# Kernel optimization log

Measured on AMD Instinct MI355X. Metric: run time of the kernel, lower is better.

Reference implementation:

```python
import jax, jax.numpy as jnp
import numpy as np

B, N, D = 4, 2048, 512   # batch, seq, feed_forward_size
H, DK, DV = 8, 64, 64    # heads, key_dim, value_dim
LN_EPS = 1e-5


def setup_inputs() -> dict:
    key = jax.random.key(0)
    ks = jax.random.split(key, 12)
    s = 0.02
    x = jax.random.normal(ks[0], (B, N, D), dtype=jnp.float32)
    # boolean mask, True = masked out (torch masked_fill semantics); causal
    attn_mask = ~jnp.tril(jnp.ones((N, N), dtype=bool))[None, None]
    ln_g = jnp.ones((D,), jnp.float32)
    ln_b = jnp.zeros((D,), jnp.float32)
    wq = jax.random.normal(ks[1], (D, H * DK), jnp.float32) * s
    bq = jnp.zeros((H * DK,), jnp.float32)
    wk = jax.random.normal(ks[2], (D, H * DK), jnp.float32) * s
    bk = jnp.zeros((H * DK,), jnp.float32)
    wv = jax.random.normal(ks[3], (D, H * DV), jnp.float32) * s
    bv = jnp.zeros((H * DV,), jnp.float32)
    wo = jax.random.normal(ks[4], (H * DV, D), jnp.float32) * s
    bo = jnp.zeros((D,), jnp.float32)
    return {"x": x, "attn_mask": attn_mask, "ln_g": ln_g, "ln_b": ln_b,
            "wq": wq, "bq": bq, "wk": wk, "bk": bk, "wv": wv, "bv": bv,
            "wo": wo, "bo": bo}


def _layernorm(x, g, b):
    mu = jnp.mean(x, axis=-1, keepdims=True)
    var = jnp.mean(jnp.square(x - mu), axis=-1, keepdims=True)
    return (x - mu) * jax.lax.rsqrt(var + LN_EPS) * g + b


def reference(x, attn_mask, ln_g, ln_b, wq, bq, wk, bk, wv, bv, wo, bo):
    xn = _layernorm(x, ln_g, ln_b)
    scale = DK ** -0.5
    q = (xn @ wq + bq).reshape(B, N, H, DK).transpose(0, 2, 1, 3) * scale  # b h n d
    k = (xn @ wk + bk).reshape(B, N, H, DK).transpose(0, 2, 1, 3)
    v = (xn @ wv + bv).reshape(B, N, H, DV).transpose(0, 2, 1, 3)
    sim = jnp.einsum('bhid,bhjd->bhij', q, k)
    sim = jnp.where(attn_mask, -jnp.finfo(sim.dtype).max, sim)
    attn = jax.nn.softmax(sim, axis=-1)  # dropout p=0 (eval)
    out = jnp.einsum('bhij,bhjd->bhid', attn, v)
    out = out.transpose(0, 2, 1, 3).reshape(B, N, H * DV)  # b n (h d)
    return out @ wo + bo
```

## Files before the change

kernel.cpp:

```cpp
#include <hip/hip_runtime.h>

typedef unsigned short u16;
typedef unsigned long long u64;
typedef __bf16 bf16x8 __attribute__((ext_vector_type(8)));
typedef float f32x4 __attribute__((ext_vector_type(4)));
typedef float f32x16 __attribute__((ext_vector_type(16)));

#define H_HEADS 8
#define DHEAD 64
#define NSEQ 2048
#define DMODEL 512
#define BATCH 4
#define MROWS (BATCH * NSEQ)
#define BH (BATCH * H_HEADS)

__device__ __forceinline__ u16 f2bf(float f) {
  unsigned u = __builtin_bit_cast(unsigned, f);
  u += 0x7fffu + ((u >> 16) & 1u);
  return (u16)(u >> 16);
}

__device__ __forceinline__ bf16x8 ldfrag(const u16* p) {
  return __builtin_bit_cast(bf16x8, *(const uint4*)p);
}

typedef __attribute__((address_space(1))) void GV;
typedef __attribute__((address_space(3))) void LV;
__device__ __forceinline__ void gld16(const void* g, void* l) {
  __builtin_amdgcn_global_load_lds((GV*)g, (LV*)l, 16, 0, 0);
}

__global__ __launch_bounds__(256) void ln_kernel(
    const float* __restrict__ x, const float* __restrict__ g,
    const float* __restrict__ b, u16* __restrict__ xn) {
  const int row = blockIdx.x;
  const int t = threadIdx.x;
  const float2 v = *(const float2*)(x + (size_t)row * DMODEL + t * 2);
  float s = v.x + v.y;
  float ss = v.x * v.x + v.y * v.y;
  #pragma unroll
  for (int d = 1; d < 64; d <<= 1) {
    s += __shfl_xor(s, d);
    ss += __shfl_xor(ss, d);
  }
  __shared__ float red[8];
  const int wave = t >> 6, lane = t & 63;
  if (lane == 0) { red[wave] = s; red[4 + wave] = ss; }
  __syncthreads();
  s = red[0] + red[1] + red[2] + red[3];
  ss = red[4] + red[5] + red[6] + red[7];
  const float mean = s * (1.0f / DMODEL);
  const float var = ss * (1.0f / DMODEL) - mean * mean;
  const float rstd = rsqrtf(var + 1e-5f);
  const float2 gg = *(const float2*)(g + t * 2);
  const float2 bb = *(const float2*)(b + t * 2);
  const float o0 = (v.x - mean) * rstd * gg.x + bb.x;
  const float o1 = (v.y - mean) * rstd * gg.y + bb.y;
  const unsigned packed = (unsigned)f2bf(o0) | ((unsigned)f2bf(o1) << 16);
  *(unsigned*)(xn + (size_t)row * DMODEL + t * 2) = packed;
}

__global__ __launch_bounds__(256) void transpose_w4_kernel(
    const float* __restrict__ w0, const float* __restrict__ w1,
    const float* __restrict__ w2, const float* __restrict__ w3,
    u16* __restrict__ WT) {
  __shared__ float tile[32][33];
  const int z = blockIdx.z;
  const float* W = (z == 0) ? w0 : (z == 1) ? w1 : (z == 2) ? w2 : w3;
  u16* dst = WT + (size_t)z * DMODEL * DMODEL;
  const int n0 = blockIdx.x * 32, k0 = blockIdx.y * 32;
  const int t = threadIdx.x;
  #pragma unroll
  for (int p = 0; p < 4; ++p) {
    const int u = p * 256 + t;
    const int r = u >> 5, c = u & 31;
    tile[r][c] = W[(size_t)(k0 + r) * DMODEL + n0 + c];
  }
  __syncthreads();
  #pragma unroll
  for (int p = 0; p < 4; ++p) {
    const int u = p * 256 + t;
    const int rn = u >> 5, ck = u & 31;
    dst[(size_t)(n0 + rn) * DMODEL + k0 + ck] = f2bf(tile[ck][rn]);
  }
}

template <int MODE>
__global__ __launch_bounds__(256) void gemm128_kernel(
    const u16* __restrict__ A, const u16* __restrict__ BT,
    const float* __restrict__ bq, const float* __restrict__ bk,
    const float* __restrict__ bv,
    u16* __restrict__ qb, u16* __restrict__ kb, u16* __restrict__ vtb,
    float* __restrict__ fout, int K) {
  __shared__ u16 lds_a[128 * 64];
  __shared__ u16 lds_b[128 * 64];
  const int t = threadIdx.x;
  const int lane = t & 63, wave = t >> 6;
  const int wm = wave >> 1, wn = wave & 1;
  const int lo = lane & 15, hi = lane >> 4;
  const int m0 = blockIdx.y * 128, n0 = blockIdx.x * 128;
  const int sr = lane >> 3;
  const int scol = (((lane & 7) ^ sr) * 8);
  f32x4 acc[4][4] = {};
  for (int k0 = 0; k0 < K; k0 += 64) {
    #pragma unroll
    for (int j = 0; j < 4; ++j) {
      const int ch = wave * 4 + j;
      gld16(A + (size_t)(m0 + ch * 8 + sr) * K + k0 + scol, lds_a + ch * 512);
      gld16(BT + (size_t)(n0 + ch * 8 + sr) * K + k0 + scol, lds_b + ch * 512);
    }
    __syncthreads();
    #pragma unroll
    for (int kc = 0; kc < 2; ++kc) {
      bf16x8 af[4], bfr[4];
      const int sw = ((lo & 7) * 8);
      #pragma unroll
      for (int i = 0; i < 4; ++i)
        af[i] = ldfrag(lds_a + (wm * 64 + i * 16 + lo) * 64 + ((kc * 32 + hi * 8) ^ sw));
      #pragma unroll
      for (int i = 0; i < 4; ++i)
        bfr[i] = ldfrag(lds_b + (wn * 64 + i * 16 + lo) * 64 + ((kc * 32 + hi * 8) ^ sw));
      __builtin_amdgcn_s_setprio(1);
      #pragma unroll
      for (int mi = 0; mi < 4; ++mi)
        #pragma unroll
        for (int ni = 0; ni < 4; ++ni)
          acc[mi][ni] = __builtin_amdgcn_mfma_f32_16x16x32_bf16(
              af[mi], bfr[ni], acc[mi][ni], 0, 0, 0);
      __builtin_amdgcn_s_setprio(0);
    }
    __syncthreads();
  }
  #pragma unroll
  for (int mi = 0; mi < 4; ++mi) {
    #pragma unroll
    for (int ni = 0; ni < 4; ++ni) {
      const int col = n0 + wn * 64 + ni * 16 + lo;
      if (MODE == 0) {
        const int mat = col >> 9, w = col & 511;
        const int hh = w >> 6, dk = w & 63;
        const float bi = (mat == 0 ? bq : (mat == 1 ? bk : bv))[w];
        const int row0 = m0 + wm * 64 + mi * 16 + hi * 4;
        const int bbx = row0 >> 11, seq0 = row0 & 2047;
        if (mat == 2) {
          u64 pk = 0;
          #pragma unroll
          for (int r = 0; r < 4; ++r)
            pk |= (u64)f2bf(acc[mi][ni][r] + bi) << (16 * r);
          *(u64*)(vtb + ((size_t)(bbx * H_HEADS + hh) * DHEAD + dk) * NSEQ + seq0) = pk;
        } else {
          const float sc = (mat == 0) ? 0.18033688f : 1.0f;
          u16* dst = (mat == 0 ? qb : kb);
          #pragma unroll
          for (int r = 0; r < 4; ++r)
            dst[(((size_t)(bbx * H_HEADS + hh) * NSEQ) + seq0 + r) * DHEAD + dk] =
                f2bf((acc[mi][ni][r] + bi) * sc);
        }
      } else {
        const float bi = bq[col];
        #pragma unroll
        for (int r = 0; r < 4; ++r) {
          const int row = m0 + wm * 64 + mi * 16 + hi * 4 + r;
          fout[(size_t)row * DMODEL + col] = acc[mi][ni][r] + bi;
        }
      }
    }
  }
}

__global__ __launch_bounds__(256, 2) void attn_kernel(
    const u16* __restrict__ Q, const u16* __restrict__ K,
    const u16* __restrict__ VT, u16* __restrict__ O) {
  __shared__ u16 lds_k[2][4096];
  __shared__ u16 lds_v[2][4096];
  const int t = threadIdx.x;
  const int lane = t & 63, wave = t >> 6;
  const int l31 = lane & 31, hi = lane >> 5;
  const int l7 = lane & 7;

  const int n = blockIdx.x;
  const int s_id = n >> 8, g = n & 255;
  const int u_id = g >> 4, q_id = g & 15;
  const int ist = (s_id & 1) ? (15 - q_id) : q_id;
  const int bh = u_id + 16 * s_id;
  const int b = bh >> 3, h = bh & 7;

  const u16* Qh = Q + (size_t)bh * NSEQ * DHEAD;
  const u16* Kh = K + (size_t)bh * NSEQ * DHEAD;
  const u16* Vh = VT + (size_t)bh * DHEAD * NSEQ;

  const int q0w = ist * 128 + wave * 32;
  const int nt = 2 * ist + 2;
  const int lastkt = (q0w + 31) >> 6;
  const int qrow = q0w + l31;

  bf16x8 qf[4];
  #pragma unroll
  for (int c = 0; c < 4; ++c)
    qf[c] = ldfrag(Qh + (size_t)qrow * DHEAD + c * 16 + hi * 8);

  f32x16 o0 = {}, o1 = {};
  float m = -INFINITY, l = 0.0f;

  const int sr = lane >> 3;
  const int scol = ((lane & 7) ^ sr) * 8;
  const int swz = l7 * 8;

  #pragma unroll
  for (int j = 0; j < 2; ++j) {
    const int ch = wave * 2 + j;
    gld16(Kh + (size_t)(ch * 8 + sr) * DHEAD + scol, lds_k[0] + ch * 512);
    gld16(Vh + (size_t)(ch * 8 + sr) * NSEQ + scol, lds_v[0] + ch * 512);
  }

  for (int kt = 0; kt < nt; ++kt) {
    const int cur = kt & 1;
    if (kt + 1 < nt) {
      const int kvn = (kt + 1) * 64;
      #pragma unroll
      for (int j = 0; j < 2; ++j) {
        const int ch = wave * 2 + j;
        gld16(Kh + (size_t)(kvn + ch * 8 + sr) * DHEAD + scol, lds_k[cur ^ 1] + ch * 512);
        gld16(Vh + (size_t)(ch * 8 + sr) * NSEQ + kvn + scol, lds_v[cur ^ 1] + ch * 512);
      }
      asm volatile("s_waitcnt vmcnt(4)" ::: "memory");
    } else {
      asm volatile("s_waitcnt vmcnt(0)" ::: "memory");
    }
    __builtin_amdgcn_s_barrier();
    __builtin_amdgcn_sched_barrier(0);

    if (kt <= lastkt) {
      const u16* lk = lds_k[cur];
      const u16* lv = lds_v[cur];
      f32x16 st0 = {}, st1 = {};

      __builtin_amdgcn_s_setprio(1);
      #pragma unroll
      for (int c = 0; c < 4; ++c) {
        const int col = (c * 16 + hi * 8) ^ swz;
        bf16x8 kf0 = ldfrag(lk + l31 * 64 + col);
        bf16x8 kf1 = ldfrag(lk + (32 + l31) * 64 + col);
        st0 = __builtin_amdgcn_mfma_f32_32x32x16_bf16(kf0, qf[c], st0, 0, 0, 0);
        st1 = __builtin_amdgcn_mfma_f32_32x32x16_bf16(kf1, qf[c], st1, 0, 0, 0);
      }
      __builtin_amdgcn_s_setprio(0);

      if (kt == lastkt) {
        const int kvb = kt * 64 + 4 * hi;
        #pragma unroll
        for (int r = 0; r < 16; ++r) {
          const int kv = kvb + (r & 3) + 8 * (r >> 2);
          if (kv > qrow) st0[r] = -1e30f;
          if (kv + 32 > qrow) st1[r] = -1e30f;
        }
      }

      float pm = st0[0];
      #pragma unroll
      for (int r = 1; r < 16; ++r) pm = fmaxf(pm, st0[r]);
      #pragma unroll
      for (int r = 0; r < 16; ++r) pm = fmaxf(pm, st1[r]);
      pm = fmaxf(pm, __shfl_xor(pm, 32));
      const float mn = fmaxf(m, pm);
      const float sc = exp2f(m - mn);
      m = mn;
      float ps = 0.0f;
      #pragma unroll
      for (int r = 0; r < 16; ++r) { st0[r] = exp2f(st0[r] - mn); ps += st0[r]; }
      #pragma unroll
      for (int r = 0; r < 16; ++r) { st1[r] = exp2f(st1[r] - mn); ps += st1[r]; }
      ps += __shfl_xor(ps, 32);
      l = l * sc + ps;
      #pragma unroll
      for (int r = 0; r < 16; ++r) { o0[r] *= sc; o1[r] *= sc; }

      bf16x8 pf0, pf1, pf2, pf3;
      {
        unsigned w0, w1, w2, w3, w4, w5, w6, w7;
        asm("v_cvt_pk_bf16_f32 %0, %1, %2" : "=v"(w0) : "v"(st0[0]), "v"(st0[1]));
        asm("v_cvt_pk_bf16_f32 %0, %1, %2" : "=v"(w1) : "v"(st0[2]), "v"(st0[3]));
        asm("v_cvt_pk_bf16_f32 %0, %1, %2" : "=v"(w2) : "v"(st0[4]), "v"(st0[5]));
        asm("v_cvt_pk_bf16_f32 %0, %1, %2" : "=v"(w3) : "v"(st0[6]), "v"(st0[7]));
        asm("v_cvt_pk_bf16_f32 %0, %1, %2" : "=v"(w4) : "v"(st0[8]), "v"(st0[9]));
        asm("v_cvt_pk_bf16_f32 %0, %1, %2" : "=v"(w5) : "v"(st0[10]), "v"(st0[11]));
        asm("v_cvt_pk_bf16_f32 %0, %1, %2" : "=v"(w6) : "v"(st0[12]), "v"(st0[13]));
        asm("v_cvt_pk_bf16_f32 %0, %1, %2" : "=v"(w7) : "v"(st0[14]), "v"(st0[15]));
        asm("v_permlane32_swap_b32 %0, %1" : "+v"(w0), "+v"(w2));
        asm("v_permlane32_swap_b32 %0, %1" : "+v"(w1), "+v"(w3));
        asm("v_permlane32_swap_b32 %0, %1" : "+v"(w4), "+v"(w6));
        asm("v_permlane32_swap_b32 %0, %1" : "+v"(w5), "+v"(w7));
        union Uu { unsigned u[4]; bf16x8 v; };
        Uu a; a.u[0] = w0; a.u[1] = w1; a.u[2] = w2; a.u[3] = w3; pf0 = a.v;
        Uu bb; bb.u[0] = w4; bb.u[1] = w5; bb.u[2] = w6; bb.u[3] = w7; pf1 = bb.v;
      }
      {
        unsigned w0, w1, w2, w3, w4, w5, w6, w7;
        asm("v_cvt_pk_bf16_f32 %0, %1, %2" : "=v"(w0) : "v"(st1[0]), "v"(st1[1]));
        asm("v_cvt_pk_bf16_f32 %0, %1, %2" : "=v"(w1) : "v"(st1[2]), "v"(st1[3]));
        asm("v_cvt_pk_bf16_f32 %0, %1, %2" : "=v"(w2) : "v"(st1[4]), "v"(st1[5]));
        asm("v_cvt_pk_bf16_f32 %0, %1, %2" : "=v"(w3) : "v"(st1[6]), "v"(st1[7]));
        asm("v_cvt_pk_bf16_f32 %0, %1, %2" : "=v"(w4) : "v"(st1[8]), "v"(st1[9]));
        asm("v_cvt_pk_bf16_f32 %0, %1, %2" : "=v"(w5) : "v"(st1[10]), "v"(st1[11]));
        asm("v_cvt_pk_bf16_f32 %0, %1, %2" : "=v"(w6) : "v"(st1[12]), "v"(st1[13]));
        asm("v_cvt_pk_bf16_f32 %0, %1, %2" : "=v"(w7) : "v"(st1[14]), "v"(st1[15]));
        asm("v_permlane32_swap_b32 %0, %1" : "+v"(w0), "+v"(w2));
        asm("v_permlane32_swap_b32 %0, %1" : "+v"(w1), "+v"(w3));
        asm("v_permlane32_swap_b32 %0, %1" : "+v"(w4), "+v"(w6));
        asm("v_permlane32_swap_b32 %0, %1" : "+v"(w5), "+v"(w7));
        union Uu { unsigned u[4]; bf16x8 v; };
        Uu a; a.u[0] = w0; a.u[1] = w1; a.u[2] = w2; a.u[3] = w3; pf2 = a.v;
        Uu bb; bb.u[0] = w4; bb.u[1] = w5; bb.u[2] = w6; bb.u[3] = w7; pf3 = bb.v;
      }

      __builtin_amdgcn_s_setprio(1);
      #pragma unroll
      for (int c = 0; c < 4; ++c) {
        const int col = (c * 16 + hi * 8) ^ swz;
        bf16x8 vf0 = ldfrag(lv + l31 * 64 + col);
        bf16x8 vf1 = ldfrag(lv + (32 + l31) * 64 + col);
        const bf16x8 pc = (c == 0) ? pf0 : (c == 1) ? pf1 : (c == 2) ? pf2 : pf3;
        o0 = __builtin_amdgcn_mfma_f32_32x32x16_bf16(vf0, pc, o0, 0, 0, 0);
        o1 = __builtin_amdgcn_mfma_f32_32x32x16_bf16(vf1, pc, o1, 0, 0, 0);
      }
      __builtin_amdgcn_s_setprio(0);
    }
    __builtin_amdgcn_sched_barrier(0);
    __builtin_amdgcn_s_barrier();
    __builtin_amdgcn_sched_barrier(0);
  }

  const float rl = __builtin_amdgcn_rcpf(l);
  u16* Ob = O + ((size_t)b * NSEQ + qrow) * DMODEL + h * DHEAD;
  #pragma unroll
  for (int d = 0; d < 2; ++d) {
    #pragma unroll
    for (int mq = 0; mq < 4; ++mq) {
      u64 pk = 0;
      #pragma unroll
      for (int c3 = 0; c3 < 4; ++c3) {
        const float v = (d ? o1[mq * 4 + c3] : o0[mq * 4 + c3]) * rl;
        pk |= (u64)f2bf(v) << (16 * c3);
      }
      *(u64*)(Ob + d * 32 + mq * 8 + hi * 4) = pk;
    }
  }
}

extern "C" void kernel_launch(void* const* d_in, const int* in_sizes, int n_in,
                              void* d_out, int out_size, void* d_ws, size_t ws_size,
                              hipStream_t stream) {
  const float* x = (const float*)d_in[0];
  const float* ln_g = (const float*)d_in[2];
  const float* ln_b = (const float*)d_in[3];
  const float* wq = (const float*)d_in[4];
  const float* bq = (const float*)d_in[5];
  const float* wk = (const float*)d_in[6];
  const float* bk = (const float*)d_in[7];
  const float* wv = (const float*)d_in[8];
  const float* bv = (const float*)d_in[9];
  const float* wo = (const float*)d_in[10];
  const float* bo = (const float*)d_in[11];

  char* ws = (char*)d_ws;
  u16* xn = (u16*)ws;     ws += (size_t)MROWS * DMODEL * 2;
  u16* wqkvT = (u16*)ws;  ws += (size_t)4 * DMODEL * DMODEL * 2;
  u16* woT = wqkvT + (size_t)3 * DMODEL * DMODEL;
  u16* qb = (u16*)ws;     ws += (size_t)MROWS * DMODEL * 2;
  u16* kb = (u16*)ws;     ws += (size_t)MROWS * DMODEL * 2;
  u16* vtb = (u16*)ws;    ws += (size_t)MROWS * DMODEL * 2;
  u16* attnb = (u16*)ws;  ws += (size_t)MROWS * DMODEL * 2;

  ln_kernel<<<MROWS, 256, 0, stream>>>(x, ln_g, ln_b, xn);
  transpose_w4_kernel<<<dim3(16, 16, 4), 256, 0, stream>>>(wq, wk, wv, wo, wqkvT);

  gemm128_kernel<0><<<dim3(12, 64), 256, 0, stream>>>(
      xn, wqkvT, bq, bk, bv, qb, kb, vtb, nullptr, DMODEL);

  attn_kernel<<<512, 256, 0, stream>>>(qb, kb, vtb, attnb);

  gemm128_kernel<1><<<dim3(4, 64), 256, 0, stream>>>(
      attnb, woT, bo, nullptr, nullptr, nullptr, nullptr, nullptr,
      (float*)d_out, DMODEL);
}
```

Before: 111.6 us.

## Split causal attention along KV into chunks with a separate merge kernel

Each causal query tile's KV range is split into up to four chunks of eight KV tiles, so the grid grows from 512 to 1280 blocks of roughly equal work. Tiles with more than one chunk write unnormalised fp32 partial outputs plus running max and sum to workspace, and a new merge kernel combines them into the bf16 attention output. Launch bounds are raised to allow four blocks per CU. The goal is better load balance and occupancy on the causal triangle. The cost is extra fp32 traffic for the partials, an additional kernel launch, and possible register pressure from the tighter launch bound.

```diff
diff --git a/kernel.cpp b/kernel.cpp
--- a/kernel.cpp
+++ b/kernel.cpp
@@ -168,9 +168,10 @@
   }
 }
 
-__global__ __launch_bounds__(256, 2) void attn_kernel(
+__global__ __launch_bounds__(256, 4) void attn_kernel(
     const u16* __restrict__ Q, const u16* __restrict__ K,
-    const u16* __restrict__ VT, u16* __restrict__ O) {
+    const u16* __restrict__ VT, u16* __restrict__ O,
+    float* __restrict__ pO, float* __restrict__ pML) {
   __shared__ u16 lds_k[2][4096];
   __shared__ u16 lds_v[2][4096];
   const int t = threadIdx.x;
@@ -179,18 +180,23 @@
   const int l7 = lane & 7;
 
   const int n = blockIdx.x;
-  const int s_id = n >> 8, g = n & 255;
-  const int u_id = g >> 4, q_id = g & 15;
-  const int ist = (s_id & 1) ? (15 - q_id) : q_id;
-  const int bh = u_id + 16 * s_id;
+  const int bh = n / 40;
+  const int r = n % 40;
+  int qt, ck, C;
+  if (r < 4)       { qt = r;                 C = 1; ck = 0; }
+  else if (r < 12) { qt = 4 + ((r - 4) >> 1);  C = 2; ck = (r - 4) & 1; }
+  else if (r < 24) { qt = 8 + (r - 12) / 3;    C = 3; ck = (r - 12) % 3; }
+  else             { qt = 12 + ((r - 24) >> 2); C = 4; ck = (r - 24) & 3; }
+  const int T = 2 * qt + 2;
+  const int kc0 = ck * 8;
+  const int L = min(8, T - kc0);
+
   const int b = bh >> 3, h = bh & 7;
-
   const u16* Qh = Q + (size_t)bh * NSEQ * DHEAD;
   const u16* Kh = K + (size_t)bh * NSEQ * DHEAD;
   const u16* Vh = VT + (size_t)bh * DHEAD * NSEQ;
 
-  const int q0w = ist * 128 + wave * 32;
-  const int nt = 2 * ist + 2;
+  const int q0w = qt * 128 + wave * 32;
   const int lastkt = (q0w + 31) >> 6;
   const int qrow = q0w + l31;
 
@@ -209,14 +215,15 @@
   #pragma unroll
   for (int j = 0; j < 2; ++j) {
     const int ch = wave * 2 + j;
-    gld16(Kh + (size_t)(ch * 8 + sr) * DHEAD + scol, lds_k[0] + ch * 512);
-    gld16(Vh + (size_t)(ch * 8 + sr) * NSEQ + scol, lds_v[0] + ch * 512);
-  }
-
-  for (int kt = 0; kt < nt; ++kt) {
-    const int cur = kt & 1;
-    if (kt + 1 < nt) {
-      const int kvn = (kt + 1) * 64;
+    gld16(Kh + (size_t)(kc0 * 64 + ch * 8 + sr) * DHEAD + scol, lds_k[0] + ch * 512);
+    gld16(Vh + (size_t)(ch * 8 + sr) * NSEQ + kc0 * 64 + scol, lds_v[0] + ch * 512);
+  }
+
+  for (int lt = 0; lt < L; ++lt) {
+    const int gk = kc0 + lt;
+    const int cur = lt & 1;
+    if (lt + 1 < L) {
+      const int kvn = (gk + 1) * 64;
       #pragma unroll
       for (int j = 0; j < 2; ++j) {
         const int ch = wave * 2 + j;
@@ -230,7 +237,7 @@
     __builtin_amdgcn_s_barrier();
     __builtin_amdgcn_sched_barrier(0);
 
-    if (kt <= lastkt) {
+    if (gk <= lastkt) {
       const u16* lk = lds_k[cur];
       const u16* lv = lds_v[cur];
       f32x16 st0 = {}, st1 = {};
@@ -246,34 +253,34 @@
       }
       __builtin_amdgcn_s_setprio(0);
 
-      if (kt == lastkt) {
-        const int kvb = kt * 64 + 4 * hi;
+      if (gk == lastkt) {
+        const int kvb = gk * 64 + 4 * hi;
         #pragma unroll
-        for (int r = 0; r < 16; ++r) {
-          const int kv = kvb + (r & 3) + 8 * (r >> 2);
-          if (kv > qrow) st0[r] = -1e30f;
-          if (kv + 32 > qrow) st1[r] = -1e30f;
+        for (int rr = 0; rr < 16; ++rr) {
+          const int kv = kvb + (rr & 3) + 8 * (rr >> 2);
+          if (kv > qrow) st0[rr] = -1e30f;
+          if (kv + 32 > qrow) st1[rr] = -1e30f;
         }
       }
 
       float pm = st0[0];
       #pragma unroll
-      for (int r = 1; r < 16; ++r) pm = fmaxf(pm, st0[r]);
-      #pragma unroll
-      for (int r = 0; r < 16; ++r) pm = fmaxf(pm, st1[r]);
+      for (int rr = 1; rr < 16; ++rr) pm = fmaxf(pm, st0[rr]);
+      #pragma unroll
+      for (int rr = 0; rr < 16; ++rr) pm = fmaxf(pm, st1[rr]);
       pm = fmaxf(pm, __shfl_xor(pm, 32));
       const float mn = fmaxf(m, pm);
       const float sc = exp2f(m - mn);
       m = mn;
       float ps = 0.0f;
       #pragma unroll
-      for (int r = 0; r < 16; ++r) { st0[r] = exp2f(st0[r] - mn); ps += st0[r]; }
-      #pragma unroll
-      for (int r = 0; r < 16; ++r) { st1[r] = exp2f(st1[r] - mn); ps += st1[r]; }
+      for (int rr = 0; rr < 16; ++rr) { st0[rr] = exp2f(st0[rr] - mn); ps += st0[rr]; }
+      #pragma unroll
+      for (int rr = 0; rr < 16; ++rr) { st1[rr] = exp2f(st1[rr] - mn); ps += st1[rr]; }
       ps += __shfl_xor(ps, 32);
       l = l * sc + ps;
       #pragma unroll
-      for (int r = 0; r < 16; ++r) { o0[r] *= sc; o1[r] *= sc; }
+      for (int rr = 0; rr < 16; ++rr) { o0[rr] *= sc; o1[rr] *= sc; }
 
       bf16x8 pf0, pf1, pf2, pf3;
       {
@@ -330,20 +337,93 @@
     __builtin_amdgcn_sched_barrier(0);
   }
 
-  const float rl = __builtin_amdgcn_rcpf(l);
-  u16* Ob = O + ((size_t)b * NSEQ + qrow) * DMODEL + h * DHEAD;
-  #pragma unroll
-  for (int d = 0; d < 2; ++d) {
+  if (C == 1) {
+    const float rl = __builtin_amdgcn_rcpf(l);
+    u16* Ob = O + ((size_t)b * NSEQ + qrow) * DMODEL + h * DHEAD;
+    #pragma unroll
+    for (int d = 0; d < 2; ++d) {
+      #pragma unroll
+      for (int mq = 0; mq < 4; ++mq) {
+        u64 pk = 0;
+        #pragma unroll
+        for (int c3 = 0; c3 < 4; ++c3) {
+          const float v = (d ? o1[mq * 4 + c3] : o0[mq * 4 + c3]) * rl;
+          pk |= (u64)f2bf(v) << (16 * c3);
+        }
+        *(u64*)(Ob + d * 32 + mq * 8 + hi * 4) = pk;
+      }
+    }
+  } else {
+    const int rloc = wave * 32 + l31;
+    float* po = pO + (size_t)n * (128 * 64) + (size_t)rloc * 64;
     #pragma unroll
     for (int mq = 0; mq < 4; ++mq) {
-      u64 pk = 0;
-      #pragma unroll
-      for (int c3 = 0; c3 < 4; ++c3) {
-        const float v = (d ? o1[mq * 4 + c3] : o0[mq * 4 + c3]) * rl;
-        pk |= (u64)f2bf(v) << (16 * c3);
-      }
-      *(u64*)(Ob + d * 32 + mq * 8 + hi * 4) = pk;
-    }
+      f32x4 v0 = {o0[mq * 4], o0[mq * 4 + 1], o0[mq * 4 + 2], o0[mq * 4 + 3]};
+      *(f32x4*)(po + mq * 8 + hi * 4) = v0;
+      f32x4 v1 = {o1[mq * 4], o1[mq * 4 + 1], o1[mq * 4 + 2], o1[mq * 4 + 3]};
+      *(f32x4*)(po + 32 + mq * 8 + hi * 4) = v1;
+    }
+    if (hi == 0) {
+      pML[(size_t)n * 256 + rloc] = m;
+      pML[(size_t)n * 256 + 128 + rloc] = l;
+    }
+  }
+}
+
+__global__ __launch_bounds__(256) void attn_merge_kernel(
+    const float* __restrict__ pO, const float* __restrict__ pML,
+    u16* __restrict__ O) {
+  const int u = blockIdx.x;
+  const int bh = u / 12, qi = u % 12;
+  const int qt = 4 + qi;
+  const int C = (qt >> 2) + 1;
+  int off;
+  if (qt < 8) off = 4 + 2 * (qt - 4);
+  else if (qt < 12) off = 12 + 3 * (qt - 8);
+  else off = 24 + 4 * (qt - 12);
+  const int slot0 = bh * 40 + off;
+  const int t = threadIdx.x;
+  const int row = t >> 1, db = (t & 1) * 32;
+
+  float mc[4], lc[4];
+  #pragma unroll
+  for (int c = 0; c < 4; ++c) {
+    if (c < C) {
+      mc[c] = pML[(size_t)(slot0 + c) * 256 + row];
+      lc[c] = pML[(size_t)(slot0 + c) * 256 + 128 + row];
+    } else { mc[c] = -INFINITY; lc[c] = 0.0f; }
+  }
+  float ms = fmaxf(fmaxf(mc[0], mc[1]), fmaxf(mc[2], mc[3]));
+  float w[4], ls = 0.0f;
+  #pragma unroll
+  for (int c = 0; c < 4; ++c) {
+    w[c] = (c < C) ? exp2f(mc[c] - ms) : 0.0f;
+    ls += w[c] * lc[c];
+  }
+  const float rl = __builtin_amdgcn_rcpf(ls);
+
+  f32x4 a[8] = {};
+  #pragma unroll
+  for (int c = 0; c < 4; ++c) {
+    if (c < C) {
+      const float* src = pO + (size_t)(slot0 + c) * (128 * 64) + (size_t)row * 64 + db;
+      const float wc = w[c];
+      #pragma unroll
+      for (int k = 0; k < 8; ++k) {
+        const f32x4 v = *(const f32x4*)(src + k * 4);
+        a[k] += v * wc;
+      }
+    }
+  }
+  const int b = bh >> 3, h = bh & 7;
+  u16* dst = O + ((size_t)b * NSEQ + qt * 128 + row) * DMODEL + h * DHEAD + db;
+  #pragma unroll
+  for (int k = 0; k < 8; k += 1) {
+    u64 pk = 0;
+    #pragma unroll
+    for (int j = 0; j < 4; ++j)
+      pk |= (u64)f2bf(a[k][j] * rl) << (16 * j);
+    *(u64*)(dst + k * 4) = pk;
   }
 }
 
@@ -370,6 +450,8 @@
   u16* kb = (u16*)ws;     ws += (size_t)MROWS * DMODEL * 2;
   u16* vtb = (u16*)ws;    ws += (size_t)MROWS * DMODEL * 2;
   u16* attnb = (u16*)ws;  ws += (size_t)MROWS * DMODEL * 2;
+  float* pO = (float*)ws; ws += (size_t)1280 * 128 * 64 * 4;
+  float* pML = (float*)ws; ws += (size_t)1280 * 256 * 4;
 
   ln_kernel<<<MROWS, 256, 0, stream>>>(x, ln_g, ln_b, xn);
   transpose_w4_kernel<<<dim3(16, 16, 4), 256, 0, stream>>>(wq, wk, wv, wo, wqkvT);
@@ -377,7 +459,8 @@
   gemm128_kernel<0><<<dim3(12, 64), 256, 0, stream>>>(
       xn, wqkvT, bq, bk, bv, qb, kb, vtb, nullptr, DMODEL);
 
-  attn_kernel<<<512, 256, 0, stream>>>(qb, kb, vtb, attnb);
+  attn_kernel<<<1280, 256, 0, stream>>>(qb, kb, vtb, attnb, pO, pML);
+  attn_merge_kernel<<<384, 256, 0, stream>>>(pO, pML, attnb);
 
   gemm128_kernel<1><<<dim3(4, 64), 256, 0, stream>>>(
       attnb, woT, bo, nullptr, nullptr, nullptr, nullptr, nullptr,
```

New measurement: 112.4 us. About the same (+0.7%).
